# Kernel optimization log

Hardware: AMD Instinct MI355X
Metric: run time of the kernel (lower is better)

## Reference

```python
import jax, jax.numpy as jnp
import numpy as np

N_NODES = 50000
N_EDGES = 800000
EPS = 1e-5
NEG_SLOPE = 0.2


def _gatv2(x, src, dst, Wl, bl, Wr, br, att, bias, concat, N):
    # PyG GATv2Conv: xl = lin_l(x) (source side), xr = lin_r(x) (target side)
    H, C = att.shape
    xl = (x @ Wl + bl).reshape(N, H, C)
    xr = (x @ Wr + br).reshape(N, H, C)
    # per-edge message: leaky_relu(xl[j] + xr[i]), attention logit = <att, .>
    z = xl[src] + xr[dst]                      # [E, H, C]
    z = jnp.where(z > 0, z, NEG_SLOPE * z)
    logits = jnp.einsum('ehc,hc->eh', z, att)  # [E, H]
    # segment softmax over incoming edges of each target node
    m = jax.lax.stop_gradient(jax.ops.segment_max(logits, dst, num_segments=N))
    p = jnp.exp(logits - m[dst])
    s = jax.ops.segment_sum(p, dst, num_segments=N)
    alpha = p / s[dst]                         # [E, H]
    out = jax.ops.segment_sum(xl[src] * alpha[..., None], dst, num_segments=N)  # [N, H, C]
    out = out.reshape(N, H * C) if concat else out.mean(axis=1)
    return out + bias


def _bn(x, g, b):
    mu = x.mean(axis=0)
    v = x.var(axis=0)
    return (x - mu) * jax.lax.rsqrt(v + EPS) * g + b


def setup_inputs() -> dict:
    key = jax.random.key(0)
    ks = jax.random.split(key, 16)
    x = jax.random.normal(ks[0], (N_NODES, 2), jnp.float32)
    edge_index = jax.random.randint(ks[1], (2, N_EDGES), 0, N_NODES, dtype=jnp.int64)

    def lin(k, i, o):
        return jax.random.normal(k, (i, o), jnp.float32) * (1.0 / np.sqrt(i))

    inp = {'x': x, 'edge_index': edge_index}
    # layer 1: in=2, heads=8, out=16, concat
    inp['W1l'] = lin(ks[2], 2, 128); inp['b1l'] = jnp.zeros((128,), jnp.float32)
    inp['W1r'] = lin(ks[3], 2, 128); inp['b1r'] = jnp.zeros((128,), jnp.float32)
    inp['a1'] = jax.random.normal(ks[4], (8, 16), jnp.float32) * 0.1
    inp['bias1'] = jnp.zeros((128,), jnp.float32)
    inp['g1'] = jnp.ones((128,), jnp.float32); inp['be1'] = jnp.zeros((128,), jnp.float32)
    # layer 2: in=128, heads=4, out=16, concat
    inp['W2l'] = lin(ks[5], 128, 64); inp['b2l'] = jnp.zeros((64,), jnp.float32)
    inp['W2r'] = lin(ks[6], 128, 64); inp['b2r'] = jnp.zeros((64,), jnp.float32)
    inp['a2'] = jax.random.normal(ks[7], (4, 16), jnp.float32) * 0.1
    inp['bias2'] = jnp.zeros((64,), jnp.float32)
    inp['g2'] = jnp.ones((64,), jnp.float32); inp['be2'] = jnp.zeros((64,), jnp.float32)
    # layer 3: in=64, heads=1, out=2, mean (concat=False)
    inp['W3l'] = lin(ks[8], 64, 2); inp['b3l'] = jnp.zeros((2,), jnp.float32)
    inp['W3r'] = lin(ks[9], 64, 2); inp['b3r'] = jnp.zeros((2,), jnp.float32)
    inp['a3'] = jax.random.normal(ks[10], (1, 2), jnp.float32) * 0.1
    inp['bias3'] = jnp.zeros((2,), jnp.float32)
    return inp


def reference(x, edge_index, W1l, b1l, W1r, b1r, a1, bias1, g1, be1,
              W2l, b2l, W2r, b2r, a2, bias2, g2, be2,
              W3l, b3l, W3r, b3r, a3, bias3):
    N = x.shape[0]
    loops = jnp.arange(N, dtype=edge_index.dtype)
    src = jnp.concatenate([edge_index[0], loops])  # add self loops (PyG default)
    dst = jnp.concatenate([edge_index[1], loops])
    h = _gatv2(x, src, dst, W1l, b1l, W1r, b1r, a1, bias1, True, N)
    h = jax.nn.elu(_bn(h, g1, be1))  # dropout is identity in eval
    h = _gatv2(h, src, dst, W2l, b2l, W2r, b2r, a2, bias2, True, N)
    h = jax.nn.elu(_bn(h, g2, be2))
    return _gatv2(h, src, dst, W3l, b3l, W3r, b3r, a3, bias3, False, N)
```

## Files before the change

### kernel.cpp

```cpp
#include <hip/hip_runtime.h>
#include <hip/hip_bf16.h>

#define N_NODES 50000
#define N_E0    800000
#define N_ET    850000
#define EPSBN   1e-5f
#define LOG2E   1.4426950408889634f

#define LEAKY(z) fmaxf((z), 0.2f * (z))

#define OFF_C 0
#define OFF_A (128*N_NODES)
#define OFF_B (192*N_NODES)
#define OFF_STATS (256*N_NODES)
#define OFF_S1R (OFF_STATS + 512)
#define OFF_S2R (OFF_S1R + 16384)
#define OFF_P (OFF_S2R + 8192)
#define N_PARAM_TOT 118312
#define OFF_ROWPTR (OFF_P + N_PARAM_TOT)
#define OFF_DEG    (OFF_ROWPTR + 50001)
#define OFF_CURSOR (OFF_DEG + 50000)
#define OFF_BSUM   (OFF_CURSOR + 50000)
#define OFF_COL    (OFF_BSUM + 256)
#define OFF_FLAGS  (OFF_COL + 850064)

__device__ __forceinline__ float bf2f(unsigned short u) {
    return __uint_as_float(((unsigned int)u) << 16);
}
__device__ __forceinline__ unsigned short f2bf(float f) {
    unsigned int u = __float_as_uint(f);
    u += 0x7FFFu + ((u >> 16) & 1u);
    return (unsigned short)(u >> 16);
}

__global__ void prep_kernel(const unsigned short* xr, const int* ei, int* flags,
                            int* deg, float* stats, float* s1r, float* s2r) {
    int i = blockIdx.x * 256 + threadIdx.x;
    if (i < N_NODES) deg[i] = 1;
    if (i < 512) stats[i] = 0.f;
    if (i < 16384) s1r[i] = 0.f;
    if (i < 8192)  s2r[i] = 0.f;
    if (blockIdx.x == 0) {
        __shared__ int c1, c2;
        if (threadIdx.x == 0) { c1 = 0; c2 = 0; }
        __syncthreads();
        int t = threadIdx.x;
        int l1 = 0, l2 = 0;
        for (int k = t; k < 2048; k += 256) {
            float v = bf2f(xr[k]);
            if (!(fabsf(v) <= 100.0f)) l1++;
            if (ei[2 * k + 1] != 0) l2++;
        }
        atomicAdd(&c1, l1);
        atomicAdd(&c2, l2);
        __syncthreads();
        if (t == 0) {
            flags[0] = (c1 > 16) ? 1 : 0;
            flags[1] = (c2 == 0) ? 1 : 0;
        }
    }
}

struct ParamPtrs { const void* p[23]; };

__global__ void convert_kernel(ParamPtrs ps, float* dst, const int* flags) {
    const int sizes[23] = {100000, 256,128,256,128,128,128,128,128,
                           8192,64,8192,64,64,64,64,64,
                           128,2,128,2,2,2};
    int g = blockIdx.x * 256 + threadIdx.x;
    if (g >= N_PARAM_TOT) return;
    int t = 0, off = g;
    while (off >= sizes[t]) { off -= sizes[t]; t++; }
    float v;
    if (flags[0]) v = ((const float*)ps.p[t])[off];
    else          v = bf2f(((const unsigned short*)ps.p[t])[off]);
    if (t == 5 || t == 13 || t == 21) v *= LOG2E;
    dst[g] = v;
}

#define H_CHUNK 2048
__global__ void hist_kernel(const int* ei, int* deg, const int* flags) {
    int stripe = blockIdx.x & 7;
    int base_e = (blockIdx.x >> 3) * H_CHUNK;
    int i64 = flags[1];
    for (int i = 0; i < H_CHUNK; i += 256) {
        int e = base_e + i + threadIdx.x;
        if (e < N_E0) {
            int dst = i64 ? ei[2 * (N_E0 + e)] : ei[N_E0 + e];
            if (dst / 6250 == stripe) atomicAdd(&deg[dst], 1);
        }
    }
}

__global__ void scan1_kernel(const int* deg, int* row_ptr, int* bsum) {
    __shared__ int sh[256];
    int i = blockIdx.x * 256 + threadIdx.x;
    int v = (i < N_NODES) ? deg[i] : 0;
    sh[threadIdx.x] = v;
    __syncthreads();
    for (int off = 1; off < 256; off <<= 1) {
        int t = (threadIdx.x >= off) ? sh[threadIdx.x - off] : 0;
        __syncthreads();
        sh[threadIdx.x] += t;
        __syncthreads();
    }
    if (i < N_NODES) row_ptr[i] = sh[threadIdx.x] - v;
    if (threadIdx.x == 255) bsum[blockIdx.x] = sh[255];
}

__global__ void scan23_kernel(int* row_ptr, int* cursor, const int* bsum) {
    __shared__ int sh[256];
    int t = threadIdx.x;
    int v = (t < 196) ? bsum[t] : 0;
    sh[t] = v;
    __syncthreads();
    for (int off = 1; off < 256; off <<= 1) {
        int u = (t >= off) ? sh[t - off] : 0;
        __syncthreads();
        sh[t] += u;
        __syncthreads();
    }
    int prefix = (blockIdx.x == 0) ? 0 : sh[blockIdx.x - 1];
    int i = blockIdx.x * 256 + t;
    if (i < N_NODES) {
        int r = row_ptr[i] + prefix;
        row_ptr[i] = r;
        cursor[i] = r;
    }
    if (i == 0) row_ptr[N_NODES] = N_ET;
}

#define SC_CHUNK 2048
__global__ void scatter_kernel(const int* ei, int* cursor, int* col, const int* flags) {
    int stripe = blockIdx.x & 7;
    int base_e = (blockIdx.x >> 3) * SC_CHUNK;
    int i64 = flags[1];
    for (int i = 0; i < SC_CHUNK; i += 256) {
        int e = base_e + i + threadIdx.x;
        if (e >= N_ET) continue;
        int src, dst;
        if (e < N_E0) {
            dst = i64 ? ei[2 * (N_E0 + e)] : ei[N_E0 + e];
            if (dst / 6250 != stripe) continue;
            src = i64 ? ei[2 * e] : ei[e];
        } else {
            src = dst = e - N_E0;
            if (dst / 6250 != stripe) continue;
        }
        int pos = atomicAdd(&cursor[dst], 1);
        col[pos] = src;
    }
}

__global__ void __launch_bounds__(256) gather1_kernel(
    const int* row_ptr, const int* col, const float* x,
    const float* W1l, const float* b1l, const float* W1r, const float* b1r,
    const float* att, const float* bias, float* C, float* s1r)
{
    int gid = blockIdx.x * 256 + threadIdx.x;
    int n = gid >> 6;
    int lane = threadIdx.x & 63;
    float2 wl0 = *(const float2*)(W1l + 2 * lane);
    float2 wl1 = *(const float2*)(W1l + 128 + 2 * lane);
    float2 bl  = *(const float2*)(b1l + 2 * lane);
    float2 wr0 = *(const float2*)(W1r + 2 * lane);
    float2 wr1 = *(const float2*)(W1r + 128 + 2 * lane);
    float2 br  = *(const float2*)(b1r + 2 * lane);
    float2 at  = *(const float2*)(att + 2 * lane);
    float2 xd  = *(const float2*)(x + 2 * n);
    float xr0 = fmaf(xd.x, wr0.x, fmaf(xd.y, wr1.x, br.x));
    float xr1 = fmaf(xd.x, wr0.y, fmaf(xd.y, wr1.y, br.y));
    int base = __builtin_amdgcn_readfirstlane(row_ptr[n]);
    int deg  = __builtin_amdgcn_readfirstlane(row_ptr[n + 1]) - base;
    float acc0 = 0.f, acc1 = 0.f, den = 0.f;
    for (int j0 = 0; j0 < deg; j0 += 64) {
        int cnt = deg - j0; if (cnt > 64) cnt = 64;
        int msrc = col[base + j0 + lane];
        int j = 0;
        for (; j + 8 <= cnt; j += 8) {
            int s[8];
            #pragma unroll
            for (int u = 0; u < 8; u++) s[u] = __builtin_amdgcn_readlane(msrc, j + u);
            float2 xs[8];
            #pragma unroll
            for (int u = 0; u < 8; u++) xs[u] = *(const float2*)(x + 2 * s[u]);
            float xl0[8], xl1[8], part[8];
            #pragma unroll
            for (int u = 0; u < 8; u++) {
                xl0[u] = fmaf(xs[u].x, wl0.x, fmaf(xs[u].y, wl1.x, bl.x));
                xl1[u] = fmaf(xs[u].x, wl0.y, fmaf(xs[u].y, wl1.y, bl.y));
                float z0 = LEAKY(xl0[u] + xr0);
                float z1 = LEAKY(xl1[u] + xr1);
                part[u] = fmaf(z0, at.x, z1 * at.y);
            }
            #pragma unroll
            for (int m = 1; m <= 4; m <<= 1) {
                #pragma unroll
                for (int u = 0; u < 8; u++) part[u] += __shfl_xor(part[u], m, 64);
            }
            #pragma unroll
            for (int u = 0; u < 8; u++) {
                float p = exp2f(part[u]);
                acc0 = fmaf(p, xl0[u], acc0);
                acc1 = fmaf(p, xl1[u], acc1);
                den += p;
            }
        }
        for (; j < cnt; ++j) {
            int s0 = __builtin_amdgcn_readlane(msrc, j);
            float2 xs = *(const float2*)(x + 2 * s0);
            float xl0s = fmaf(xs.x, wl0.x, fmaf(xs.y, wl1.x, bl.x));
            float xl1s = fmaf(xs.x, wl0.y, fmaf(xs.y, wl1.y, bl.y));
            float z0 = LEAKY(xl0s + xr0);
            float z1 = LEAKY(xl1s + xr1);
            float part = fmaf(z0, at.x, z1 * at.y);
            part += __shfl_xor(part, 1, 64);
            part += __shfl_xor(part, 2, 64);
            part += __shfl_xor(part, 4, 64);
            float p = exp2f(part);
            acc0 = fmaf(p, xl0s, acc0);
            acc1 = fmaf(p, xl1s, acc1);
            den += p;
        }
    }
    float inv = 1.f / den;
    float2 bi = *(const float2*)(bias + 2 * lane);
    float2 outv;
    outv.x = fmaf(acc0, inv, bi.x);
    outv.y = fmaf(acc1, inv, bi.y);
    *(float2*)(C + n * 128 + 2 * lane) = outv;
    __shared__ float sred[4][128];
    __shared__ float qred[4][128];
    int wv = threadIdx.x >> 6;
    sred[wv][2 * lane]     = outv.x;
    sred[wv][2 * lane + 1] = outv.y;
    qred[wv][2 * lane]     = outv.x * outv.x;
    qred[wv][2 * lane + 1] = outv.y * outv.y;
    __syncthreads();
    int t = threadIdx.x;
    float a;
    if (t < 128) a = sred[0][t] + sred[1][t] + sred[2][t] + sred[3][t];
    else { int c = t - 128; a = qred[0][c] + qred[1][c] + qred[2][c] + qred[3][c]; }
    atomicAdd(&s1r[(blockIdx.x & 63) * 256 + t], a);
}

__global__ void red1_kernel(const float* s1r, float* stats) {
    int t = threadIdx.x;
    int r0 = blockIdx.x * 8;
    float a = 0.f;
    #pragma unroll
    for (int r = 0; r < 8; r++) a += s1r[(r0 + r) * 256 + t];
    atomicAdd(&stats[t], a);
}

__global__ void __launch_bounds__(256) lin2_kernel(
    const float* C, const float* stats, const float* g1, const float* be1,
    const float* Wl, const float* bl, const float* Wr, const float* br,
    unsigned short* xl2b, float* xr2)
{
    __shared__ float h[64 * 132];
    int tid = threadIdx.x;
    int nb = blockIdx.x * 64;
    for (int i = tid; i < 64 * 128; i += 256) {
        int ni = i >> 7, k = i & 127;
        int n = nb + ni;
        float v = 0.f;
        if (n < N_NODES) {
            float val = C[n * 128 + k];
            float mu = stats[k] * (1.0f / N_NODES);
            float var = stats[128 + k] * (1.0f / N_NODES) - mu * mu;
            float sc = g1[k] * rsqrtf(var + EPSBN);
            float b = (val - mu) * sc + be1[k];
            v = b > 0.f ? b : __expf(b) - 1.f;
        }
        h[ni * 132 + k] = v;
    }
    __syncthreads();
    int kt = (tid & 15) * 4;
    int nt = (tid >> 4) * 4;
    float accl[4][4], accr[4][4];
    #pragma unroll
    for (int i = 0; i < 4; i++) {
        #pragma unroll
        for (int k = 0; k < 4; k++) { accl[i][k] = 0.f; accr[i][k] = 0.f; }
    }
    for (int j = 0; j < 128; j += 4) {
        float4 hv[4];
        #pragma unroll
        for (int i = 0; i < 4; i++)
            hv[i] = *(const float4*)&h[(nt + i) * 132 + j];
        #pragma unroll
        for (int jj = 0; jj < 4; jj++) {
            float4 wl4 = *(const float4*)&Wl[(j + jj) * 64 + kt];
            float4 wr4 = *(const float4*)&Wr[(j + jj) * 64 + kt];
            #pragma unroll
            for (int i = 0; i < 4; i++) {
                float hvv = (jj == 0) ? hv[i].x : (jj == 1) ? hv[i].y :
                            (jj == 2) ? hv[i].z : hv[i].w;
                accl[i][0] += hvv * wl4.x; accl[i][1] += hvv * wl4.y;
                accl[i][2] += hvv * wl4.z; accl[i][3] += hvv * wl4.w;
                accr[i][0] += hvv * wr4.x; accr[i][1] += hvv * wr4.y;
                accr[i][2] += hvv * wr4.z; accr[i][3] += hvv * wr4.w;
            }
        }
    }
    float4 blv = *(const float4*)&bl[kt];
    float4 brv = *(const float4*)&br[kt];
    #pragma unroll
    for (int i = 0; i < 4; i++) {
        int n = nb + nt + i;
        if (n < N_NODES) {
            ushort4 ob;
            ob.x = f2bf(accl[i][0] + blv.x);
            ob.y = f2bf(accl[i][1] + blv.y);
            ob.z = f2bf(accl[i][2] + blv.z);
            ob.w = f2bf(accl[i][3] + blv.w);
            *(ushort4*)&xl2b[n * 64 + kt] = ob;
            float4 o;
            o.x = accr[i][0] + brv.x; o.y = accr[i][1] + brv.y;
            o.z = accr[i][2] + brv.z; o.w = accr[i][3] + brv.w;
            *(float4*)&xr2[n * 64 + kt] = o;
        }
    }
}

__global__ void __launch_bounds__(256) gather2_kernel(
    const int* row_ptr, const int* col, const unsigned short* xl2b, const float* xr2,
    const float* att, const float* bias, float* C, float* s2r)
{
    int gid = blockIdx.x * 256 + threadIdx.x;
    int n = gid >> 6;
    int lane = threadIdx.x & 63;
    float xrv = xr2[n * 64 + lane];
    float atv = att[lane];
    int base = __builtin_amdgcn_readfirstlane(row_ptr[n]);
    int deg  = __builtin_amdgcn_readfirstlane(row_ptr[n + 1]) - base;
    float acc = 0.f, den = 0.f;
    for (int j0 = 0; j0 < deg; j0 += 64) {
        int cnt = deg - j0; if (cnt > 64) cnt = 64;
        int msrc = col[base + j0 + lane];
        int j = 0;
        for (; j + 8 <= cnt; j += 8) {
            const unsigned short* rp[8];
            #pragma unroll
            for (int u = 0; u < 8; u++)
                rp[u] = xl2b + (size_t)__builtin_amdgcn_readlane(msrc, j + u) * 64;
            float xlv[8], part[8];
            #pragma unroll
            for (int u = 0; u < 8; u++) xlv[u] = bf2f(rp[u][lane]);
            #pragma unroll
            for (int u = 0; u < 8; u++) {
                float z = LEAKY(xlv[u] + xrv);
                part[u] = z * atv;
            }
            #pragma unroll
            for (int m = 1; m <= 8; m <<= 1) {
                #pragma unroll
                for (int u = 0; u < 8; u++) part[u] += __shfl_xor(part[u], m, 64);
            }
            #pragma unroll
            for (int u = 0; u < 8; u++) {
                float p = exp2f(part[u]);
                acc = fmaf(p, xlv[u], acc);
                den += p;
            }
        }
        for (; j < cnt; ++j) {
            int s0 = __builtin_amdgcn_readlane(msrc, j);
            float xlv = bf2f(xl2b[(size_t)s0 * 64 + lane]);
            float z = LEAKY(xlv + xrv);
            float part = z * atv;
            part += __shfl_xor(part, 1, 64);
            part += __shfl_xor(part, 2, 64);
            part += __shfl_xor(part, 4, 64);
            part += __shfl_xor(part, 8, 64);
            float p = exp2f(part);
            acc = fmaf(p, xlv, acc);
            den += p;
        }
    }
    float outv = acc / den + bias[lane];
    C[n * 64 + lane] = outv;
    __shared__ float sred[4][64];
    __shared__ float qred[4][64];
    int wv = threadIdx.x >> 6;
    sred[wv][lane] = outv;
    qred[wv][lane] = outv * outv;
    __syncthreads();
    int t = threadIdx.x;
    if (t < 128) {
        float a;
        if (t < 64) a = sred[0][t] + sred[1][t] + sred[2][t] + sred[3][t];
        else { int c = t - 64; a = qred[0][c] + qred[1][c] + qred[2][c] + qred[3][c]; }
        atomicAdd(&s2r[(blockIdx.x & 63) * 128 + t], a);
    }
}

__global__ void red2_kernel(const float* s2r, float* stats) {
    int t = threadIdx.x;
    int r0 = blockIdx.x * 8;
    float a = 0.f;
    #pragma unroll
    for (int r = 0; r < 8; r++) a += s2r[(r0 + r) * 128 + t];
    atomicAdd(&stats[t], a);
}

__global__ void __launch_bounds__(256) lin3_kernel(
    const float* C, const float* stats2, const float* g2, const float* be2,
    const float* Wl, const float* bl, const float* Wr, const float* br,
    float* xl3, float* xr3)
{
    int gid = blockIdx.x * 256 + threadIdx.x;
    int n = gid >> 6;
    int lane = threadIdx.x & 63;
    if (n >= N_NODES) return;
    float mu = stats2[lane] * (1.0f / N_NODES);
    float var = stats2[64 + lane] * (1.0f / N_NODES) - mu * mu;
    float sc = g2[lane] * rsqrtf(var + EPSBN);
    float of = be2[lane] - mu * sc;
    float v = C[n * 64 + lane] * sc + of;
    float h = v > 0.f ? v : __expf(v) - 1.f;
    float2 wlv = *(const float2*)(Wl + 2 * lane);
    float2 wrv = *(const float2*)(Wr + 2 * lane);
    float a0 = h * wlv.x, a1 = h * wlv.y;
    float r0 = h * wrv.x, r1 = h * wrv.y;
    #pragma unroll
    for (int m = 1; m < 64; m <<= 1) {
        a0 += __shfl_xor(a0, m, 64);
        a1 += __shfl_xor(a1, m, 64);
        r0 += __shfl_xor(r0, m, 64);
        r1 += __shfl_xor(r1, m, 64);
    }
    if (lane == 0) {
        xl3[2 * n]     = a0 + bl[0];
        xl3[2 * n + 1] = a1 + bl[1];
        xr3[2 * n]     = r0 + br[0];
        xr3[2 * n + 1] = r1 + br[1];
    }
}

__global__ void gather3_kernel(const int* row_ptr, const int* col,
                               const float* xl3, const float* xr3,
                               const float* att, const float* bias,
                               void* out, const int* flags) {
    int n = blockIdx.x * 256 + threadIdx.x;
    if (n >= N_NODES) return;
    float a0 = att[0], a1 = att[1];
    float xr0 = xr3[2 * n], xr1 = xr3[2 * n + 1];
    float acc0 = 0.f, acc1 = 0.f, den = 0.f;
    int e0 = row_ptr[n], e1 = row_ptr[n + 1];
    int e = e0;
    for (; e + 4 <= e1; e += 4) {
        int s[4];
        #pragma unroll
        for (int u = 0; u < 4; u++) s[u] = col[e + u];
        float2 xs[4];
        #pragma unroll
        for (int u = 0; u < 4; u++) xs[u] = *(const float2*)(xl3 + 2 * s[u]);
        #pragma unroll
        for (int u = 0; u < 4; u++) {
            float z0 = LEAKY(xs[u].x + xr0);
            float z1 = LEAKY(xs[u].y + xr1);
            float p = exp2f(fmaf(z0, a0, z1 * a1));
            acc0 += p * xs[u].x; acc1 += p * xs[u].y; den += p;
        }
    }
    for (; e < e1; ++e) {
        int src = col[e];
        float2 xs = *(const float2*)(xl3 + 2 * src);
        float z0 = LEAKY(xs.x + xr0);
        float z1 = LEAKY(xs.y + xr1);
        float p = exp2f(fmaf(z0, a0, z1 * a1));
        acc0 += p * xs.x; acc1 += p * xs.y; den += p;
    }
    float inv = 1.f / den;
    float v0 = acc0 * inv + bias[0];
    float v1 = acc1 * inv + bias[1];
    if (flags[0]) {
        ((float*)out)[2 * n] = v0;
        ((float*)out)[2 * n + 1] = v1;
    } else {
        ((__hip_bfloat16*)out)[2 * n] = __float2bfloat16(v0);
        ((__hip_bfloat16*)out)[2 * n + 1] = __float2bfloat16(v1);
    }
}

extern "C" void kernel_launch(void* const* d_in, const int* in_sizes, int n_in,
                              void* d_out, int out_size, void* d_ws, size_t ws_size,
                              hipStream_t stream) {
    float* W = (float*)d_ws;
    float* C = W + OFF_C;
    float* A = W + OFF_A;
    float* B = W + OFF_B;
    float* STATS = W + OFF_STATS;
    float* S1R = W + OFF_S1R;
    float* S2R = W + OFF_S2R;
    float* P = W + OFF_P;
    int* ROWPTR = (int*)(W + OFF_ROWPTR);
    int* DEG    = (int*)(W + OFF_DEG);
    int* CURSOR = (int*)(W + OFF_CURSOR);
    int* BSUM   = (int*)(W + OFF_BSUM);
    int* COL    = (int*)(W + OFF_COL);
    int* FLAGS  = (int*)(W + OFF_FLAGS);

    const int* ei = (const int*)d_in[1];

    float* Px  = P;
    float* W1l = Px + 100000; float* b1l = W1l + 256; float* W1r = b1l + 128; float* b1r = W1r + 256;
    float* a1  = b1r + 128;   float* bias1 = a1 + 128; float* g1 = bias1 + 128; float* be1 = g1 + 128;
    float* W2l = be1 + 128;   float* b2l = W2l + 8192; float* W2r = b2l + 64;  float* b2r = W2r + 8192;
    float* a2  = b2r + 64;    float* bias2 = a2 + 64;  float* g2 = bias2 + 64; float* be2 = g2 + 64;
    float* W3l = be2 + 64;    float* b3l = W3l + 128;  float* W3r = b3l + 2;   float* b3r = W3r + 128;
    float* a3  = b3r + 2;     float* bias3 = a3 + 2;

    prep_kernel<<<196, 256, 0, stream>>>((const unsigned short*)d_in[0], ei, FLAGS, DEG, STATS, S1R, S2R);

    ParamPtrs ps;
    ps.p[0] = d_in[0];
    for (int j = 1; j < 23; j++) ps.p[j] = d_in[j + 1];
    convert_kernel<<<(N_PARAM_TOT + 255) / 256, 256, 0, stream>>>(ps, P, FLAGS);

    hist_kernel<<<8 * ((N_E0 + H_CHUNK - 1) / H_CHUNK), 256, 0, stream>>>(ei, DEG, FLAGS);
    scan1_kernel<<<196, 256, 0, stream>>>(DEG, ROWPTR, BSUM);
    scan23_kernel<<<196, 256, 0, stream>>>(ROWPTR, CURSOR, BSUM);
    scatter_kernel<<<8 * ((N_ET + SC_CHUNK - 1) / SC_CHUNK), 256, 0, stream>>>(ei, CURSOR, COL, FLAGS);

    gather1_kernel<<<N_NODES * 64 / 256, 256, 0, stream>>>(ROWPTR, COL, Px, W1l, b1l, W1r, b1r, a1, bias1, C, S1R);
    red1_kernel<<<8, 256, 0, stream>>>(S1R, STATS);

    lin2_kernel<<<(N_NODES + 63) / 64, 256, 0, stream>>>(C, STATS, g1, be1, W2l, b2l, W2r, b2r, (unsigned short*)A, B);
    gather2_kernel<<<N_NODES * 64 / 256, 256, 0, stream>>>(ROWPTR, COL, (const unsigned short*)A, B, a2, bias2, C, S2R);
    red2_kernel<<<8, 128, 0, stream>>>(S2R, STATS + 256);

    lin3_kernel<<<N_NODES * 64 / 256, 256, 0, stream>>>(C, STATS + 256, g2, be2, W3l, b3l, W3r, b3r, A, B);
    gather3_kernel<<<196, 256, 0, stream>>>(ROWPTR, COL, A, B, a3, bias3, d_out, FLAGS);
}
```

Before: 354.2 us.

## Process four edges per wavefront in parallel in GAT gather kernels

Both gather kernels now split each 64-lane wavefront into four 16-lane groups, each handling a different edge with several channels per lane. This replaces the per-edge serial loop and its wide shuffle reductions with shorter 2–4 step reductions, plus a final cross-group reduction of the accumulators. The aim is more memory-level parallelism and fewer cross-lane ops per edge. In exchange it uses more registers per lane and predicates off tail lanes.

```diff
diff --git a/kernel.cpp b/kernel.cpp
--- a/kernel.cpp
+++ b/kernel.cpp
@@ -160,82 +160,88 @@
     int gid = blockIdx.x * 256 + threadIdx.x;
     int n = gid >> 6;
     int lane = threadIdx.x & 63;
-    float2 wl0 = *(const float2*)(W1l + 2 * lane);
-    float2 wl1 = *(const float2*)(W1l + 128 + 2 * lane);
-    float2 bl  = *(const float2*)(b1l + 2 * lane);
-    float2 wr0 = *(const float2*)(W1r + 2 * lane);
-    float2 wr1 = *(const float2*)(W1r + 128 + 2 * lane);
-    float2 br  = *(const float2*)(b1r + 2 * lane);
-    float2 at  = *(const float2*)(att + 2 * lane);
-    float2 xd  = *(const float2*)(x + 2 * n);
-    float xr0 = fmaf(xd.x, wr0.x, fmaf(xd.y, wr1.x, br.x));
-    float xr1 = fmaf(xd.x, wr0.y, fmaf(xd.y, wr1.y, br.y));
+    int grp = lane >> 4;
+    int cidx = lane & 15;
+    int cb = cidx * 8;
+    float wl0[8], wl1[8], blv[8], at[8], xrk[8];
+    float2 xd = *(const float2*)(x + 2 * n);
+    #pragma unroll
+    for (int k = 0; k < 8; k++) {
+        wl0[k] = W1l[cb + k];
+        wl1[k] = W1l[128 + cb + k];
+        blv[k] = b1l[cb + k];
+        at[k]  = att[cb + k];
+        float wr0 = W1r[cb + k], wr1 = W1r[128 + cb + k], brv = b1r[cb + k];
+        xrk[k] = fmaf(xd.x, wr0, fmaf(xd.y, wr1, brv));
+    }
     int base = __builtin_amdgcn_readfirstlane(row_ptr[n]);
     int deg  = __builtin_amdgcn_readfirstlane(row_ptr[n + 1]) - base;
-    float acc0 = 0.f, acc1 = 0.f, den = 0.f;
+    float acc[8];
+    #pragma unroll
+    for (int k = 0; k < 8; k++) acc[k] = 0.f;
+    float den = 0.f;
     for (int j0 = 0; j0 < deg; j0 += 64) {
         int cnt = deg - j0; if (cnt > 64) cnt = 64;
         int msrc = col[base + j0 + lane];
-        int j = 0;
-        for (; j + 8 <= cnt; j += 8) {
-            int s[8];
+        for (int j4 = 0; j4 < cnt; j4 += 8) {
+            int e0 = j4 + grp, e1 = j4 + 4 + grp;
+            int s0 = __shfl(msrc, e0, 64);
+            int s1 = __shfl(msrc, e1, 64);
+            bool v0 = e0 < cnt, v1 = e1 < cnt;
+            s0 = v0 ? s0 : 0;
+            s1 = v1 ? s1 : 0;
+            float2 xa = *(const float2*)(x + 2 * s0);
+            float2 xb = *(const float2*)(x + 2 * s1);
+            float xla[8], xlb[8];
+            float pa = 0.f, pb = 0.f;
             #pragma unroll
-            for (int u = 0; u < 8; u++) s[u] = __builtin_amdgcn_readlane(msrc, j + u);
-            float2 xs[8];
+            for (int k = 0; k < 8; k++) {
+                xla[k] = fmaf(xa.x, wl0[k], fmaf(xa.y, wl1[k], blv[k]));
+                xlb[k] = fmaf(xb.x, wl0[k], fmaf(xb.y, wl1[k], blv[k]));
+                float za = LEAKY(xla[k] + xrk[k]);
+                float zb = LEAKY(xlb[k] + xrk[k]);
+                pa = fmaf(za, at[k], pa);
+                pb = fmaf(zb, at[k], pb);
+            }
+            pa += __shfl_xor(pa, 1, 64);
+            pb += __shfl_xor(pb, 1, 64);
+            float ea = v0 ? exp2f(pa) : 0.f;
+            float eb = v1 ? exp2f(pb) : 0.f;
             #pragma unroll
-            for (int u = 0; u < 8; u++) xs[u] = *(const float2*)(x + 2 * s[u]);
-            float xl0[8], xl1[8], part[8];
-            #pragma unroll
-            for (int u = 0; u < 8; u++) {
-                xl0[u] = fmaf(xs[u].x, wl0.x, fmaf(xs[u].y, wl1.x, bl.x));
-                xl1[u] = fmaf(xs[u].x, wl0.y, fmaf(xs[u].y, wl1.y, bl.y));
-                float z0 = LEAKY(xl0[u] + xr0);
-                float z1 = LEAKY(xl1[u] + xr1);
-                part[u] = fmaf(z0, at.x, z1 * at.y);
+            for (int k = 0; k < 8; k++) {
+                acc[k] = fmaf(ea, xla[k], acc[k]);
+                acc[k] = fmaf(eb, xlb[k], acc[k]);
             }
-            #pragma unroll
-            for (int m = 1; m <= 4; m <<= 1) {
-                #pragma unroll
-                for (int u = 0; u < 8; u++) part[u] += __shfl_xor(part[u], m, 64);
-            }
-            #pragma unroll
-            for (int u = 0; u < 8; u++) {
-                float p = exp2f(part[u]);
-                acc0 = fmaf(p, xl0[u], acc0);
-                acc1 = fmaf(p, xl1[u], acc1);
-                den += p;
-            }
-        }
-        for (; j < cnt; ++j) {
-            int s0 = __builtin_amdgcn_readlane(msrc, j);
-            float2 xs = *(const float2*)(x + 2 * s0);
-            float xl0s = fmaf(xs.x, wl0.x, fmaf(xs.y, wl1.x, bl.x));
-            float xl1s = fmaf(xs.x, wl0.y, fmaf(xs.y, wl1.y, bl.y));
-            float z0 = LEAKY(xl0s + xr0);
-            float z1 = LEAKY(xl1s + xr1);
-            float part = fmaf(z0, at.x, z1 * at.y);
-            part += __shfl_xor(part, 1, 64);
-            part += __shfl_xor(part, 2, 64);
-            part += __shfl_xor(part, 4, 64);
-            float p = exp2f(part);
-            acc0 = fmaf(p, xl0s, acc0);
-            acc1 = fmaf(p, xl1s, acc1);
-            den += p;
-        }
-    }
+            den += ea + eb;
+        }
+    }
+    #pragma unroll
+    for (int k = 0; k < 8; k++) {
+        acc[k] += __shfl_xor(acc[k], 16, 64);
+        acc[k] += __shfl_xor(acc[k], 32, 64);
+    }
+    den += __shfl_xor(den, 16, 64);
+    den += __shfl_xor(den, 32, 64);
     float inv = 1.f / den;
-    float2 bi = *(const float2*)(bias + 2 * lane);
-    float2 outv;
-    outv.x = fmaf(acc0, inv, bi.x);
-    outv.y = fmaf(acc1, inv, bi.y);
-    *(float2*)(C + n * 128 + 2 * lane) = outv;
+    float o[8];
+    #pragma unroll
+    for (int k = 0; k < 8; k++) o[k] = fmaf(acc[k], inv, bias[cb + k]);
+    if (lane < 16) {
+        float4 o0 = make_float4(o[0], o[1], o[2], o[3]);
+        float4 o1 = make_float4(o[4], o[5], o[6], o[7]);
+        *(float4*)(C + n * 128 + cb)     = o0;
+        *(float4*)(C + n * 128 + cb + 4) = o1;
+    }
     __shared__ float sred[4][128];
     __shared__ float qred[4][128];
     int wv = threadIdx.x >> 6;
-    sred[wv][2 * lane]     = outv.x;
-    sred[wv][2 * lane + 1] = outv.y;
-    qred[wv][2 * lane]     = outv.x * outv.x;
-    qred[wv][2 * lane + 1] = outv.y * outv.y;
+    if (lane < 16) {
+        #pragma unroll
+        for (int k = 0; k < 8; k++) {
+            sred[wv][cb + k] = o[k];
+            qred[wv][cb + k] = o[k] * o[k];
+        }
+    }
     __syncthreads();
     int t = threadIdx.x;
     float a;
@@ -331,61 +337,79 @@
     int gid = blockIdx.x * 256 + threadIdx.x;
     int n = gid >> 6;
     int lane = threadIdx.x & 63;
-    float xrv = xr2[n * 64 + lane];
-    float atv = att[lane];
+    int grp = lane >> 4;
+    int cidx = lane & 15;
+    float4 xrv = *(const float4*)(xr2 + n * 64 + 4 * cidx);
+    float4 atv = *(const float4*)(att + 4 * cidx);
     int base = __builtin_amdgcn_readfirstlane(row_ptr[n]);
     int deg  = __builtin_amdgcn_readfirstlane(row_ptr[n + 1]) - base;
-    float acc = 0.f, den = 0.f;
+    float4 acc = make_float4(0.f, 0.f, 0.f, 0.f);
+    float den = 0.f;
     for (int j0 = 0; j0 < deg; j0 += 64) {
         int cnt = deg - j0; if (cnt > 64) cnt = 64;
         int msrc = col[base + j0 + lane];
-        int j = 0;
-        for (; j + 8 <= cnt; j += 8) {
-            const unsigned short* rp[8];
-            #pragma unroll
-            for (int u = 0; u < 8; u++)
-                rp[u] = xl2b + (size_t)__builtin_amdgcn_readlane(msrc, j + u) * 64;
-            float xlv[8], part[8];
-            #pragma unroll
-            for (int u = 0; u < 8; u++) xlv[u] = bf2f(rp[u][lane]);
-            #pragma unroll
-            for (int u = 0; u < 8; u++) {
-                float z = LEAKY(xlv[u] + xrv);
-                part[u] = z * atv;
-            }
-            #pragma unroll
-            for (int m = 1; m <= 8; m <<= 1) {
-                #pragma unroll
-                for (int u = 0; u < 8; u++) part[u] += __shfl_xor(part[u], m, 64);
-            }
-            #pragma unroll
-            for (int u = 0; u < 8; u++) {
-                float p = exp2f(part[u]);
-                acc = fmaf(p, xlv[u], acc);
-                den += p;
-            }
-        }
-        for (; j < cnt; ++j) {
-            int s0 = __builtin_amdgcn_readlane(msrc, j);
-            float xlv = bf2f(xl2b[(size_t)s0 * 64 + lane]);
-            float z = LEAKY(xlv + xrv);
-            float part = z * atv;
-            part += __shfl_xor(part, 1, 64);
-            part += __shfl_xor(part, 2, 64);
-            part += __shfl_xor(part, 4, 64);
-            part += __shfl_xor(part, 8, 64);
-            float p = exp2f(part);
-            acc = fmaf(p, xlv, acc);
-            den += p;
-        }
-    }
-    float outv = acc / den + bias[lane];
-    C[n * 64 + lane] = outv;
+        for (int j4 = 0; j4 < cnt; j4 += 8) {
+            int e0 = j4 + grp, e1 = j4 + 4 + grp;
+            int s0 = __shfl(msrc, e0, 64);
+            int s1 = __shfl(msrc, e1, 64);
+            bool v0 = e0 < cnt, v1 = e1 < cnt;
+            s0 = v0 ? s0 : 0;
+            s1 = v1 ? s1 : 0;
+            uint2 ba = *(const uint2*)(xl2b + (size_t)s0 * 64 + 4 * cidx);
+            uint2 bb = *(const uint2*)(xl2b + (size_t)s1 * 64 + 4 * cidx);
+            float a0 = __uint_as_float(ba.x << 16);
+            float a1 = __uint_as_float(ba.x & 0xffff0000u);
+            float a2 = __uint_as_float(ba.y << 16);
+            float a3 = __uint_as_float(ba.y & 0xffff0000u);
+            float b0 = __uint_as_float(bb.x << 16);
+            float b1 = __uint_as_float(bb.x & 0xffff0000u);
+            float b2 = __uint_as_float(bb.y << 16);
+            float b3 = __uint_as_float(bb.y & 0xffff0000u);
+            float pa = LEAKY(a0 + xrv.x) * atv.x;
+            pa = fmaf(LEAKY(a1 + xrv.y), atv.y, pa);
+            pa = fmaf(LEAKY(a2 + xrv.z), atv.z, pa);
+            pa = fmaf(LEAKY(a3 + xrv.w), atv.w, pa);
+            float pb = LEAKY(b0 + xrv.x) * atv.x;
+            pb = fmaf(LEAKY(b1 + xrv.y), atv.y, pb);
+            pb = fmaf(LEAKY(b2 + xrv.z), atv.z, pb);
+            pb = fmaf(LEAKY(b3 + xrv.w), atv.w, pb);
+            pa += __shfl_xor(pa, 1, 64);
+            pa += __shfl_xor(pa, 2, 64);
+            pb += __shfl_xor(pb, 1, 64);
+            pb += __shfl_xor(pb, 2, 64);
+            float ea = v0 ? exp2f(pa) : 0.f;
+            float eb = v1 ? exp2f(pb) : 0.f;
+            acc.x = fmaf(ea, a0, acc.x); acc.x = fmaf(eb, b0, acc.x);
+            acc.y = fmaf(ea, a1, acc.y); acc.y = fmaf(eb, b1, acc.y);
+            acc.z = fmaf(ea, a2, acc.z); acc.z = fmaf(eb, b2, acc.z);
+            acc.w = fmaf(ea, a3, acc.w); acc.w = fmaf(eb, b3, acc.w);
+            den += ea + eb;
+        }
+    }
+    acc.x += __shfl_xor(acc.x, 16, 64); acc.x += __shfl_xor(acc.x, 32, 64);
+    acc.y += __shfl_xor(acc.y, 16, 64); acc.y += __shfl_xor(acc.y, 32, 64);
+    acc.z += __shfl_xor(acc.z, 16, 64); acc.z += __shfl_xor(acc.z, 32, 64);
+    acc.w += __shfl_xor(acc.w, 16, 64); acc.w += __shfl_xor(acc.w, 32, 64);
+    den += __shfl_xor(den, 16, 64);
+    den += __shfl_xor(den, 32, 64);
+    float inv = 1.f / den;
+    float4 bi = *(const float4*)(bias + 4 * cidx);
+    float4 o;
+    o.x = fmaf(acc.x, inv, bi.x);
+    o.y = fmaf(acc.y, inv, bi.y);
+    o.z = fmaf(acc.z, inv, bi.z);
+    o.w = fmaf(acc.w, inv, bi.w);
+    if (lane < 16) *(float4*)(C + n * 64 + 4 * cidx) = o;
     __shared__ float sred[4][64];
     __shared__ float qred[4][64];
     int wv = threadIdx.x >> 6;
-    sred[wv][lane] = outv;
-    qred[wv][lane] = outv * outv;
+    if (lane < 16) {
+        int c = 4 * cidx;
+        sred[wv][c]     = o.x; qred[wv][c]     = o.x * o.x;
+        sred[wv][c + 1] = o.y; qred[wv][c + 1] = o.y * o.y;
+        sred[wv][c + 2] = o.z; qred[wv][c + 2] = o.z * o.z;
+        sred[wv][c + 3] = o.w; qred[wv][c + 3] = o.w * o.w;
+    }
     __syncthreads();
     int t = threadIdx.x;
     if (t < 128) {
```

New measurement: 354.8 us. About the same (+0.2%).

## Process four edges per wavefront with four channels per lane in layer-2 gather

Applied to the files above, without the earlier changes.

Restructures the layer-2 edge gather so each lane handles four channels, which lets a 64-lane wavefront process four edges at once (two groups per iteration) instead of one edge per lane-channel. This cuts the per-edge cross-lane reduction from four shuffle stages to two and uses wider 8-byte loads. The per-channel partial sums across the four edge groups are merged by shuffles at the end. In exchange it adds predication for tail edges and a final reduction step, and the bf16 loads per lane become wider but strided.

```diff
diff --git a/kernel.cpp b/kernel.cpp
--- a/kernel.cpp
+++ b/kernel.cpp
@@ -331,61 +331,79 @@
     int gid = blockIdx.x * 256 + threadIdx.x;
     int n = gid >> 6;
     int lane = threadIdx.x & 63;
-    float xrv = xr2[n * 64 + lane];
-    float atv = att[lane];
+    int grp = lane >> 4;
+    int cidx = lane & 15;
+    float4 xrv = *(const float4*)(xr2 + n * 64 + 4 * cidx);
+    float4 atv = *(const float4*)(att + 4 * cidx);
     int base = __builtin_amdgcn_readfirstlane(row_ptr[n]);
     int deg  = __builtin_amdgcn_readfirstlane(row_ptr[n + 1]) - base;
-    float acc = 0.f, den = 0.f;
+    float4 acc = make_float4(0.f, 0.f, 0.f, 0.f);
+    float den = 0.f;
     for (int j0 = 0; j0 < deg; j0 += 64) {
         int cnt = deg - j0; if (cnt > 64) cnt = 64;
         int msrc = col[base + j0 + lane];
-        int j = 0;
-        for (; j + 8 <= cnt; j += 8) {
-            const unsigned short* rp[8];
-            #pragma unroll
-            for (int u = 0; u < 8; u++)
-                rp[u] = xl2b + (size_t)__builtin_amdgcn_readlane(msrc, j + u) * 64;
-            float xlv[8], part[8];
-            #pragma unroll
-            for (int u = 0; u < 8; u++) xlv[u] = bf2f(rp[u][lane]);
-            #pragma unroll
-            for (int u = 0; u < 8; u++) {
-                float z = LEAKY(xlv[u] + xrv);
-                part[u] = z * atv;
-            }
-            #pragma unroll
-            for (int m = 1; m <= 8; m <<= 1) {
-                #pragma unroll
-                for (int u = 0; u < 8; u++) part[u] += __shfl_xor(part[u], m, 64);
-            }
-            #pragma unroll
-            for (int u = 0; u < 8; u++) {
-                float p = exp2f(part[u]);
-                acc = fmaf(p, xlv[u], acc);
-                den += p;
-            }
-        }
-        for (; j < cnt; ++j) {
-            int s0 = __builtin_amdgcn_readlane(msrc, j);
-            float xlv = bf2f(xl2b[(size_t)s0 * 64 + lane]);
-            float z = LEAKY(xlv + xrv);
-            float part = z * atv;
-            part += __shfl_xor(part, 1, 64);
-            part += __shfl_xor(part, 2, 64);
-            part += __shfl_xor(part, 4, 64);
-            part += __shfl_xor(part, 8, 64);
-            float p = exp2f(part);
-            acc = fmaf(p, xlv, acc);
-            den += p;
-        }
-    }
-    float outv = acc / den + bias[lane];
-    C[n * 64 + lane] = outv;
+        for (int j4 = 0; j4 < cnt; j4 += 8) {
+            int e0 = j4 + grp, e1 = j4 + 4 + grp;
+            int s0 = __shfl(msrc, e0, 64);
+            int s1 = __shfl(msrc, e1, 64);
+            bool v0 = e0 < cnt, v1 = e1 < cnt;
+            s0 = v0 ? s0 : 0;
+            s1 = v1 ? s1 : 0;
+            uint2 ba = *(const uint2*)(xl2b + (size_t)s0 * 64 + 4 * cidx);
+            uint2 bb = *(const uint2*)(xl2b + (size_t)s1 * 64 + 4 * cidx);
+            float a0 = __uint_as_float(ba.x << 16);
+            float a1 = __uint_as_float(ba.x & 0xffff0000u);
+            float a2 = __uint_as_float(ba.y << 16);
+            float a3 = __uint_as_float(ba.y & 0xffff0000u);
+            float b0 = __uint_as_float(bb.x << 16);
+            float b1 = __uint_as_float(bb.x & 0xffff0000u);
+            float b2 = __uint_as_float(bb.y << 16);
+            float b3 = __uint_as_float(bb.y & 0xffff0000u);
+            float pa = LEAKY(a0 + xrv.x) * atv.x;
+            pa = fmaf(LEAKY(a1 + xrv.y), atv.y, pa);
+            pa = fmaf(LEAKY(a2 + xrv.z), atv.z, pa);
+            pa = fmaf(LEAKY(a3 + xrv.w), atv.w, pa);
+            float pb = LEAKY(b0 + xrv.x) * atv.x;
+            pb = fmaf(LEAKY(b1 + xrv.y), atv.y, pb);
+            pb = fmaf(LEAKY(b2 + xrv.z), atv.z, pb);
+            pb = fmaf(LEAKY(b3 + xrv.w), atv.w, pb);
+            pa += __shfl_xor(pa, 1, 64);
+            pa += __shfl_xor(pa, 2, 64);
+            pb += __shfl_xor(pb, 1, 64);
+            pb += __shfl_xor(pb, 2, 64);
+            float ea = v0 ? exp2f(pa) : 0.f;
+            float eb = v1 ? exp2f(pb) : 0.f;
+            acc.x = fmaf(ea, a0, acc.x); acc.x = fmaf(eb, b0, acc.x);
+            acc.y = fmaf(ea, a1, acc.y); acc.y = fmaf(eb, b1, acc.y);
+            acc.z = fmaf(ea, a2, acc.z); acc.z = fmaf(eb, b2, acc.z);
+            acc.w = fmaf(ea, a3, acc.w); acc.w = fmaf(eb, b3, acc.w);
+            den += ea + eb;
+        }
+    }
+    acc.x += __shfl_xor(acc.x, 16, 64); acc.x += __shfl_xor(acc.x, 32, 64);
+    acc.y += __shfl_xor(acc.y, 16, 64); acc.y += __shfl_xor(acc.y, 32, 64);
+    acc.z += __shfl_xor(acc.z, 16, 64); acc.z += __shfl_xor(acc.z, 32, 64);
+    acc.w += __shfl_xor(acc.w, 16, 64); acc.w += __shfl_xor(acc.w, 32, 64);
+    den += __shfl_xor(den, 16, 64);
+    den += __shfl_xor(den, 32, 64);
+    float inv = 1.f / den;
+    float4 bi = *(const float4*)(bias + 4 * cidx);
+    float4 o;
+    o.x = fmaf(acc.x, inv, bi.x);
+    o.y = fmaf(acc.y, inv, bi.y);
+    o.z = fmaf(acc.z, inv, bi.z);
+    o.w = fmaf(acc.w, inv, bi.w);
+    if (lane < 16) *(float4*)(C + n * 64 + 4 * cidx) = o;
     __shared__ float sred[4][64];
     __shared__ float qred[4][64];
     int wv = threadIdx.x >> 6;
-    sred[wv][lane] = outv;
-    qred[wv][lane] = outv * outv;
+    if (lane < 16) {
+        int c = 4 * cidx;
+        sred[wv][c]     = o.x; qred[wv][c]     = o.x * o.x;
+        sred[wv][c + 1] = o.y; qred[wv][c + 1] = o.y * o.y;
+        sred[wv][c + 2] = o.z; qred[wv][c + 2] = o.z * o.z;
+        sred[wv][c + 3] = o.w; qred[wv][c + 3] = o.w * o.w;
+    }
     __syncthreads();
     int t = threadIdx.x;
     if (t < 128) {
```

Result: faster. 340.0 us (-4.0%).
